# Optimization experiments

Hardware: AMD Instinct MI355X
Metric: run time of the kernel (lower is better)

Reference implementation:

```python
import jax, jax.numpy as jnp
import numpy as np

B, N, NNZ = 512, 512, 8192
ENTITY, EMB, HID = 30000, 64, 100
PAD_ID = ENTITY - 1


def setup_inputs() -> dict:
    key = jax.random.key(0)
    ks = jax.random.split(key, 8)
    hyperneigh = jax.random.randint(ks[0], (B, N), 0, PAD_ID, dtype=jnp.int64)
    adj_rows = jax.random.randint(ks[1], (B, NNZ), 0, N, dtype=jnp.int32)
    adj_cols = jax.random.randint(ks[2], (B, NNZ), 0, N, dtype=jnp.int32)
    adj_vals = jax.random.uniform(ks[3], (B, NNZ), dtype=jnp.float32)
    emb_table = jax.random.normal(ks[4], (ENTITY, EMB), dtype=jnp.float32)
    emb_table = emb_table.at[PAD_ID].set(0.0)  # padding_idx row is zero
    stdv1 = 1.0 / np.sqrt(HID)
    W1 = jax.random.uniform(ks[5], (EMB, HID), minval=-stdv1, maxval=stdv1, dtype=jnp.float32)
    b1 = jax.random.uniform(ks[6], (HID,), minval=-stdv1, maxval=stdv1, dtype=jnp.float32)
    k7, k8 = jax.random.split(ks[7])
    W2 = jax.random.uniform(k7, (HID, HID), minval=-stdv1, maxval=stdv1, dtype=jnp.float32)
    b2 = jax.random.uniform(k8, (HID,), minval=-stdv1, maxval=stdv1, dtype=jnp.float32)
    return dict(hyperneigh=hyperneigh, adj_rows=adj_rows, adj_cols=adj_cols,
                adj_vals=adj_vals, emb_table=emb_table, W1=W1, b1=b1, W2=W2, b2=b2)


def _spmm(rows, cols, vals, X):
    # sparse [N,N] @ X[N,H] via gather + segment_sum (COO, fixed nnz)
    msgs = vals[:, None] * X[cols]  # [nnz, H]
    return jax.ops.segment_sum(msgs, rows, num_segments=N)

_batched_spmm = jax.vmap(_spmm, in_axes=(0, 0, 0, 0))


def reference(hyperneigh, adj_rows, adj_cols, adj_vals, emb_table, W1, b1, W2, b2):
    # embedding lookup: [B, N, EMB]
    x = emb_table[hyperneigh]
    # HGNN_conv layer 1: support = X @ W; out = A @ support + bias
    support = jnp.einsum('bne,eh->bnh', x, W1)
    x = _batched_spmm(adj_rows, adj_cols, adj_vals, support) + b1
    # HGNN_conv layer 2
    support = jnp.einsum('bnh,hk->bnk', x, W2)
    x = _batched_spmm(adj_rows, adj_cols, adj_vals, support) + b2
    return x  # [B, N, HID]
```

## Files before the change

### kernel.cpp

```cpp
#include <hip/hip_runtime.h>

#define BB   512
#define NN   512
#define NNZ  8192
#define EMB  64
#define HID  100
#define DUMPC 512

#define OFF_CSR_RC  0
#define OFF_CSR_V   16777216
#define OFF_ROWST   25165824
#define OFF_SUPT    26216448
#define OFF_W1T     84936704
#define OFF_W2T     84951040

typedef __attribute__((ext_vector_type(8))) short short8;
typedef __attribute__((ext_vector_type(4))) float floatx4;

__device__ __forceinline__ unsigned short f2bf(float f) {
    unsigned u = __float_as_uint(f);
    unsigned r = (u + 0x7fffu + ((u >> 16) & 1u)) >> 16;
    return (unsigned short)r;
}

__device__ __forceinline__ short8 pack8(float4 a, float4 b) {
    short8 s;
    s[0] = (short)f2bf(a.x); s[1] = (short)f2bf(a.y);
    s[2] = (short)f2bf(a.z); s[3] = (short)f2bf(a.w);
    s[4] = (short)f2bf(b.x); s[5] = (short)f2bf(b.y);
    s[6] = (short)f2bf(b.z); s[7] = (short)f2bf(b.w);
    return s;
}

__device__ __forceinline__ size_t supt_addr(int batch, int col, int k) {
    return (size_t)batch * 57344 + (size_t)(k >> 5) * 3584 + (size_t)col * 32 + (k & 31);
}

__global__ __launch_bounds__(512) void k_csr_build(
    const int* __restrict__ rows, const int* __restrict__ cols,
    const float* __restrict__ vals, int* __restrict__ row_start,
    int* __restrict__ csr_rc, unsigned short* __restrict__ csr_v,
    const float* __restrict__ W1, const float* __restrict__ W2,
    unsigned short* __restrict__ w1t, unsigned short* __restrict__ w2t)
{
    __shared__ int   rl[NNZ];
    __shared__ float vl[NNZ];
    __shared__ int   cnt[NN];
    __shared__ int   sc[NN];

    const int b   = blockIdx.x;
    const int tid = threadIdx.x;

    if (b == BB) {
        for (int id = tid; id < 112 * 128; id += 512) {
            if (id < 112 * 64) {
                int h = id >> 6, k = id & 63;
                float f = (h < 100) ? W1[k * 100 + h] : 0.f;
                w1t[id] = f2bf(f);
            }
            int h = id >> 7, k = id & 127;
            float f = (h < 100 && k < 100) ? W2[k * 100 + h] : 0.f;
            w2t[id] = f2bf(f);
        }
        return;
    }

    const int*   rb = rows + (size_t)b * NNZ;
    const int*   cb = cols + (size_t)b * NNZ;
    const float* vb = vals + (size_t)b * NNZ;

    cnt[tid] = 0;
    __syncthreads();

    #pragma unroll
    for (int i = 0; i < NNZ / 512; ++i)
        atomicAdd(&cnt[rb[tid + i * 512]], 1);
    __syncthreads();

    const int own = cnt[tid];
    sc[tid] = own;
    __syncthreads();
    #pragma unroll
    for (int off = 1; off < NN; off <<= 1) {
        int v = (tid >= off) ? sc[tid - off] : 0;
        __syncthreads();
        sc[tid] += v;
        __syncthreads();
    }
    row_start[b * 513 + tid + 1] = sc[tid];
    if (tid == 0) row_start[b * 513] = 0;
    cnt[tid] = sc[tid] - own;
    __syncthreads();

    #pragma unroll
    for (int i = 0; i < NNZ / 512; ++i) {
        int idx = tid + i * 512;
        int   r = rb[idx];
        int   c = cb[idx];
        float v = vb[idx];
        int pos = atomicAdd(&cnt[r], 1);
        rl[pos] = (r << 16) | c;
        vl[pos] = v;
    }
    __syncthreads();

    {
        const int s = sc[tid] - own;
        const int e = sc[tid];
        for (int j = s; j < e - 1; ++j) {
            int pj = rl[j];
            if ((pj & 0xffff) == DUMPC) continue;
            float add = 0.f;
            bool mod = false;
            for (int j2 = j + 1; j2 < e; ++j2) {
                if (rl[j2] == pj) {
                    add += vl[j2];
                    rl[j2] = (pj & 0xffff0000) | DUMPC;
                    mod = true;
                }
            }
            if (mod) vl[j] += add;
        }
    }
    __syncthreads();

    #pragma unroll
    for (int i = 0; i < NNZ / 512; ++i) {
        int idx = tid + i * 512;
        csr_rc[(size_t)b * NNZ + idx] = rl[idx];
        csr_v [(size_t)b * NNZ + idx] = f2bf(vl[idx]);
    }
}

__global__ __launch_bounds__(256) void k_gemm1_mfma(
    const int* __restrict__ hyper, const float* __restrict__ emb,
    const unsigned short* __restrict__ w1t, unsigned short* __restrict__ supT)
{
    const int lane = threadIdx.x & 63, wave = threadIdx.x >> 6;
    const int l15 = lane & 15, g4 = lane >> 4;

    short8 bq[7][2];
    #pragma unroll
    for (int ct = 0; ct < 7; ++ct)
        #pragma unroll
        for (int kt = 0; kt < 2; ++kt)
            bq[ct][kt] = *(const short8*)(w1t + (ct * 16 + l15) * 64 + kt * 32 + g4 * 8);

    const int wsid = blockIdx.x * 4 + wave;
    #pragma unroll 2
    for (int i = 0; i < 4; ++i) {
        const int  rb   = wsid * 4 + i;
        const long base = (long)rb * 16;
        const int  rid  = hyper[base + l15];
        const float* ep = emb + (long)rid * EMB + g4 * 8;
        float4 f0 = *(const float4*)(ep);
        float4 f1 = *(const float4*)(ep + 4);
        float4 f2 = *(const float4*)(ep + 32);
        float4 f3 = *(const float4*)(ep + 36);
        short8 a0 = pack8(f0, f1);
        short8 a1 = pack8(f2, f3);

        floatx4 acc[7];
        #pragma unroll
        for (int ct = 0; ct < 7; ++ct) acc[ct] = (floatx4)0.f;
        #pragma unroll
        for (int ct = 0; ct < 7; ++ct) {
            acc[ct] = __builtin_amdgcn_mfma_f32_16x16x32_bf16(a0, bq[ct][0], acc[ct], 0, 0, 0);
            acc[ct] = __builtin_amdgcn_mfma_f32_16x16x32_bf16(a1, bq[ct][1], acc[ct], 0, 0, 0);
        }

        const int batch = rb >> 5;
        const int inrow = (rb & 31) * 16 + g4 * 4;
        #pragma unroll
        for (int ct = 0; ct < 7; ++ct) {
            int col = ct * 16 + l15;
            uint2 w;
            w.x = (unsigned)f2bf(acc[ct][0]) | ((unsigned)f2bf(acc[ct][1]) << 16);
            w.y = (unsigned)f2bf(acc[ct][2]) | ((unsigned)f2bf(acc[ct][3]) << 16);
            *(uint2*)(supT + supt_addr(batch, col, inrow)) = w;
        }
    }
}

__global__ __launch_bounds__(256) void k_gemm2_mfma(
    const unsigned short* __restrict__ h1, const unsigned short* __restrict__ w2t,
    unsigned short* __restrict__ supT)
{
    const int lane = threadIdx.x & 63, wave = threadIdx.x >> 6;
    const int l15 = lane & 15, g4 = lane >> 4;
    const int ct0 = (wave & 1) ? 4 : 0;

    short8 bq[4][4];
    #pragma unroll
    for (int ctl = 0; ctl < 4; ++ctl) {
        int ct = ct0 + ctl;
        if (ct < 7)
            #pragma unroll
            for (int kt = 0; kt < 4; ++kt)
                bq[ctl][kt] = *(const short8*)(w2t + (ct * 16 + l15) * 128 + kt * 32 + g4 * 8);
    }

    const int wp = blockIdx.x * 2 + (wave >> 1);
    #pragma unroll 2
    for (int i = 0; i < 8; ++i) {
        const int  rb   = wp * 8 + i;
        const long base = (long)rb * 16;
        const unsigned short* rp = h1 + (size_t)(base + l15) * 112;

        short8 a[4];
        #pragma unroll
        for (int kt = 0; kt < 4; ++kt) {
            int k0 = kt * 32 + g4 * 8;
            short8 av = (short8)(short)0;
            if (k0 < 112) av = *(const short8*)(rp + k0);
            a[kt] = av;
        }

        floatx4 acc[4];
        #pragma unroll
        for (int ctl = 0; ctl < 4; ++ctl) acc[ctl] = (floatx4)0.f;
        #pragma unroll
        for (int ctl = 0; ctl < 4; ++ctl) {
            if (ct0 + ctl < 7) {
                #pragma unroll
                for (int kt = 0; kt < 4; ++kt)
                    acc[ctl] = __builtin_amdgcn_mfma_f32_16x16x32_bf16(a[kt], bq[ctl][kt], acc[ctl], 0, 0, 0);
            }
        }

        const int batch = rb >> 5;
        const int inrow = (rb & 31) * 16 + g4 * 4;
        #pragma unroll
        for (int ctl = 0; ctl < 4; ++ctl) {
            if (ct0 + ctl < 7) {
                int col = (ct0 + ctl) * 16 + l15;
                uint2 w;
                w.x = (unsigned)f2bf(acc[ctl][0]) | ((unsigned)f2bf(acc[ctl][1]) << 16);
                w.y = (unsigned)f2bf(acc[ctl][2]) | ((unsigned)f2bf(acc[ctl][3]) << 16);
                *(uint2*)(supT + supt_addr(batch, col, inrow)) = w;
            }
        }
    }
}

template<bool FINAL>
__global__ __launch_bounds__(512) void k_spmm_mfma(
    const int* __restrict__ row_st, const int* __restrict__ rc,
    const unsigned short* __restrict__ vv, const unsigned short* __restrict__ supT,
    const float* __restrict__ bias, unsigned short* __restrict__ h1,
    float* __restrict__ out)
{
    __shared__ unsigned short Ad[64 * 512 + 64];

    const int tid    = threadIdx.x;
    const int xcd    = blockIdx.x & 7;
    const int local  = blockIdx.x >> 3;
    const int batch  = xcd * 64 + (local >> 3);
    const int stripe = local & 7;
    const int r0     = stripe * 64;

    const int s0 = row_st[batch * 513 + r0];
    const int e0 = row_st[batch * 513 + r0 + 64];
    const int*            rcb = rc + (size_t)batch * NNZ;
    const unsigned short* vvb = vv + (size_t)batch * NNZ;
    int            pc[3];
    unsigned short pv[3];
    #pragma unroll
    for (int i = 0; i < 3; ++i) {
        int idx = s0 + tid + i * 512;
        bool ok = idx < e0;
        pc[i] = ok ? rcb[idx] : 0;
        pv[i] = ok ? vvb[idx] : 0;
    }

    {
        uint4* z = (uint4*)Ad;
        #pragma unroll
        for (int i = 0; i < 9; ++i) {
            int idx = tid + i * 512;
            if (idx < 4104) z[idx] = make_uint4(0u, 0u, 0u, 0u);
        }
    }
    __syncthreads();

    #pragma unroll
    for (int i = 0; i < 3; ++i) {
        int idx = s0 + tid + i * 512;
        if (idx < e0) {
            int r = ((pc[i] >> 16) & 0xffff) - r0;
            int c = pc[i] & 0xffff;
            int a = (c < 512)
                ? ((r >> 4) * 8192 + (c >> 5) * 512 + ((c >> 3) & 3) * 128 + (r & 15) * 8 + (c & 7))
                : (64 * 512 + (tid & 63));
            Ad[a] = pv[i];
        }
    }
    for (int idx = s0 + 1536 + tid; idx < e0; idx += 512) {
        int p = rcb[idx];
        int r = ((p >> 16) & 0xffff) - r0;
        int c = p & 0xffff;
        int a = (c < 512)
            ? ((r >> 4) * 8192 + (c >> 5) * 512 + ((c >> 3) & 3) * 128 + (r & 15) * 8 + (c & 7))
            : (64 * 512 + (tid & 63));
        Ad[a] = vvb[idx];
    }
    __syncthreads();

    const int lane = tid & 63, wave = tid >> 6;
    const int l15 = lane & 15, g4 = lane >> 4;
    const int ng  = wave & 3, kh = wave >> 2;
    const int nt0 = ng * 2;
    const bool two = (nt0 + 1) < 7;
    const int ktb = kh * 8;

    const unsigned short* b0p = supT + (size_t)batch * 57344 + (size_t)ktb * 3584
                               + (nt0 * 16 + l15) * 32 + g4 * 8;
    const unsigned short* b1p = b0p + 512;
    const unsigned short* ap  = Ad + (size_t)ktb * 512 + lane * 8;

    floatx4 acc[2][4];
    #pragma unroll
    for (int n = 0; n < 2; ++n)
        #pragma unroll
        for (int m = 0; m < 4; ++m) acc[n][m] = (floatx4)0.f;

    #pragma unroll 4
    for (int kt = 0; kt < 8; ++kt) {
        short8 b0 = *(const short8*)(b0p + (size_t)kt * 3584);
        short8 b1 = (short8)(short)0;
        if (two) b1 = *(const short8*)(b1p + (size_t)kt * 3584);
        #pragma unroll
        for (int m = 0; m < 4; ++m) {
            short8 a = *(const short8*)(ap + m * 8192 + kt * 512);
            acc[0][m] = __builtin_amdgcn_mfma_f32_16x16x32_bf16(a, b0, acc[0][m], 0, 0, 0);
            if (two)
                acc[1][m] = __builtin_amdgcn_mfma_f32_16x16x32_bf16(a, b1, acc[1][m], 0, 0, 0);
        }
    }
    __syncthreads();

    float* redu = (float*)Ad;
    if (kh == 1) {
        #pragma unroll
        for (int nn = 0; nn < 2; ++nn)
            #pragma unroll
            for (int m = 0; m < 4; ++m)
                #pragma unroll
                for (int q = 0; q < 4; ++q)
                    redu[ng * 2048 + ((nn * 4 + m) * 4 + q) * 64 + lane] = acc[nn][m][q];
    }
    __syncthreads();

    if (kh == 0) {
        #pragma unroll
        for (int nn = 0; nn < 2; ++nn)
            #pragma unroll
            for (int m = 0; m < 4; ++m)
                #pragma unroll
                for (int q = 0; q < 4; ++q)
                    acc[nn][m][q] += redu[ng * 2048 + ((nn * 4 + m) * 4 + q) * 64 + lane];

        if (FINAL) {
            float* st = (float*)((char*)Ad + 32768);
            #pragma unroll
            for (int nn = 0; nn < 2; ++nn) {
                int nt = nt0 + nn;
                if (nt >= 7) break;
                int col = nt * 16 + l15;
                float bi = (col < HID) ? bias[col] : 0.f;
                #pragma unroll
                for (int m = 0; m < 4; ++m) {
                    int row = m * 16 + g4 * 4;
                    #pragma unroll
                    for (int q = 0; q < 4; ++q)
                        st[(row + q) * 112 + col] = acc[nn][m][q] + bi;
                }
            }
        } else {
            unsigned short* st = (unsigned short*)((char*)Ad + 32768);
            #pragma unroll
            for (int nn = 0; nn < 2; ++nn) {
                int nt = nt0 + nn;
                if (nt >= 7) break;
                int col = nt * 16 + l15;
                float bi = (col < HID) ? bias[col] : 0.f;
                #pragma unroll
                for (int m = 0; m < 4; ++m) {
                    int row = m * 16 + g4 * 4;
                    #pragma unroll
                    for (int q = 0; q < 4; ++q)
                        st[(row + q) * 112 + col] = f2bf(acc[nn][m][q] + bi);
                }
            }
        }
    }
    __syncthreads();

    if (FINAL) {
        const float* st = (const float*)((char*)Ad + 32768);
        #pragma unroll
        for (int i = 0; i < 4; ++i) {
            int flat = tid + i * 512;
            if (flat < 1600) {
                int row = flat / 25, wi = flat - row * 25;
                float4 v = *(const float4*)(st + row * 112 + wi * 4);
                *(float4*)(out + ((size_t)batch * NN + r0 + row) * HID + wi * 4) = v;
            }
        }
    } else {
        const unsigned short* st = (const unsigned short*)((char*)Ad + 32768);
        #pragma unroll
        for (int i = 0; i < 2; ++i) {
            int flat = tid + i * 512;
            if (flat < 896) {
                int row = flat / 14, wi = flat - row * 14;
                uint4 v = *(const uint4*)(st + row * 112 + wi * 8);
                *(uint4*)(h1 + ((size_t)batch * NN + r0 + row) * 112 + wi * 8) = v;
            }
        }
    }
}

extern "C" void kernel_launch(void* const* d_in, const int* in_sizes, int n_in,
                              void* d_out, int out_size, void* d_ws, size_t ws_size,
                              hipStream_t stream)
{
    const int*   hyper = (const int*)  d_in[0];
    const int*   arows = (const int*)  d_in[1];
    const int*   acols = (const int*)  d_in[2];
    const float* avals = (const float*)d_in[3];
    const float* emb   = (const float*)d_in[4];
    const float* W1    = (const float*)d_in[5];
    const float* b1    = (const float*)d_in[6];
    const float* W2    = (const float*)d_in[7];
    const float* b2    = (const float*)d_in[8];

    float*          out = (float*)d_out;
    unsigned short* h1  = (unsigned short*)d_out;
    char*           ws  = (char*)d_ws;

    int*            csr_rc = (int*)           (ws + OFF_CSR_RC);
    unsigned short* csr_v  = (unsigned short*)(ws + OFF_CSR_V);
    int*            row_st = (int*)           (ws + OFF_ROWST);
    unsigned short* supT   = (unsigned short*)(ws + OFF_SUPT);
    unsigned short* w1t    = (unsigned short*)(ws + OFF_W1T);
    unsigned short* w2t    = (unsigned short*)(ws + OFF_W2T);

    k_csr_build<<<BB + 1, 512, 0, stream>>>(arows, acols, avals, row_st,
                                            csr_rc, csr_v, W1, W2, w1t, w2t);

    k_gemm1_mfma<<<1024, 256, 0, stream>>>(hyper, emb, w1t, supT);
    k_spmm_mfma<false><<<BB * 8, 512, 0, stream>>>(row_st, csr_rc, csr_v, supT, b1, h1, out);
    k_gemm2_mfma<<<1024, 256, 0, stream>>>(h1, w2t, supT);
    k_spmm_mfma<true><<<BB * 8, 512, 0, stream>>>(row_st, csr_rc, csr_v, supT, b2, h1, out);
}
```

Measured before the change: 238.6 us.

## Detect duplicate COO entries with shared-memory bitmap and wave-shuffle prefix scan

Replaces the per-row quadratic duplicate-merge loop in CSR build with a per-(row,col) shared bitmap set by atomicOr. Duplicates are diverted to an exception list and folded into the first occurrence via atomicAdd. The block-wide Hillis-Steele scan with many barriers becomes a wave-level shuffle scan plus an 8-wave combine. The weight-transpose block moves to block 0. This adds 32KB of LDS per block, which may lower occupancy, and the exception list has a fixed cap.

```diff
diff --git a/kernel.cpp b/kernel.cpp
--- a/kernel.cpp
+++ b/kernel.cpp
@@ -6,6 +6,7 @@
 #define EMB  64
 #define HID  100
 #define DUMPC 512
+#define EXCAP 1024
 
 #define OFF_CSR_RC  0
 #define OFF_CSR_V   16777216
@@ -43,15 +44,18 @@
     const float* __restrict__ W1, const float* __restrict__ W2,
     unsigned short* __restrict__ w1t, unsigned short* __restrict__ w2t)
 {
-    __shared__ int   rl[NNZ];
-    __shared__ float vl[NNZ];
-    __shared__ int   cnt[NN];
-    __shared__ int   sc[NN];
-
-    const int b   = blockIdx.x;
+    __shared__ int      rl[NNZ];
+    __shared__ float    vl[NNZ];
+    __shared__ unsigned bmap[NN * 16];
+    __shared__ int      cnt[NN];
+    __shared__ int      sc[NN];
+    __shared__ int      exc_rc[EXCAP];
+    __shared__ float    exc_v[EXCAP];
+    __shared__ int      wsum[8], woff[8], nexc;
+
     const int tid = threadIdx.x;
 
-    if (b == BB) {
+    if (blockIdx.x == 0) {
         for (int id = tid; id < 112 * 128; id += 512) {
             if (id < 112 * 64) {
                 int h = id >> 6, k = id & 63;
@@ -64,12 +68,16 @@
         }
         return;
     }
+    const int b = blockIdx.x - 1;
 
     const int*   rb = rows + (size_t)b * NNZ;
     const int*   cb = cols + (size_t)b * NNZ;
     const float* vb = vals + (size_t)b * NNZ;
 
     cnt[tid] = 0;
+    #pragma unroll
+    for (int i = 0; i < 16; ++i) bmap[tid + i * 512] = 0u;
+    if (tid == 0) nexc = 0;
     __syncthreads();
 
     #pragma unroll
@@ -77,19 +85,27 @@
         atomicAdd(&cnt[rb[tid + i * 512]], 1);
     __syncthreads();
 
+    const int lane = tid & 63, wid = tid >> 6;
     const int own = cnt[tid];
-    sc[tid] = own;
-    __syncthreads();
-    #pragma unroll
-    for (int off = 1; off < NN; off <<= 1) {
-        int v = (tid >= off) ? sc[tid - off] : 0;
-        __syncthreads();
-        sc[tid] += v;
-        __syncthreads();
-    }
-    row_start[b * 513 + tid + 1] = sc[tid];
+    int x = own;
+    #pragma unroll
+    for (int off = 1; off < 64; off <<= 1) {
+        int y = __shfl_up(x, off);
+        if (lane >= off) x += y;
+    }
+    if (lane == 63) wsum[wid] = x;
+    __syncthreads();
+    if (tid == 0) {
+        int a = 0;
+        #pragma unroll
+        for (int w = 0; w < 8; ++w) { woff[w] = a; a += wsum[w]; }
+    }
+    __syncthreads();
+    x += woff[wid];
+    sc[tid] = x;
+    row_start[b * 513 + tid + 1] = x;
     if (tid == 0) row_start[b * 513] = 0;
-    cnt[tid] = sc[tid] - own;
+    cnt[tid] = x - own;
     __syncthreads();
 
     #pragma unroll
@@ -98,28 +114,34 @@
         int   r = rb[idx];
         int   c = cb[idx];
         float v = vb[idx];
+        unsigned bit = 1u << (c & 31);
+        unsigned old = atomicOr(&bmap[(r << 4) + (c >> 5)], bit);
         int pos = atomicAdd(&cnt[r], 1);
-        rl[pos] = (r << 16) | c;
-        vl[pos] = v;
+        bool dup = (old & bit) != 0;
+        int e = -1;
+        if (dup) e = atomicAdd(&nexc, 1);
+        if (dup && e < EXCAP) {
+            rl[pos] = (r << 16) | DUMPC;
+            vl[pos] = 0.f;
+            exc_rc[e] = (r << 16) | c;
+            exc_v[e]  = v;
+        } else {
+            rl[pos] = (r << 16) | c;
+            vl[pos] = v;
+        }
     }
     __syncthreads();
 
     {
-        const int s = sc[tid] - own;
-        const int e = sc[tid];
-        for (int j = s; j < e - 1; ++j) {
-            int pj = rl[j];
-            if ((pj & 0xffff) == DUMPC) continue;
-            float add = 0.f;
-            bool mod = false;
-            for (int j2 = j + 1; j2 < e; ++j2) {
-                if (rl[j2] == pj) {
-                    add += vl[j2];
-                    rl[j2] = (pj & 0xffff0000) | DUMPC;
-                    mod = true;
-                }
-            }
-            if (mod) vl[j] += add;
+        int ne = nexc < EXCAP ? nexc : EXCAP;
+        for (int t = tid; t < ne; t += 512) {
+            int key = exc_rc[t];
+            int r   = key >> 16;
+            int lo  = r ? sc[r - 1] : 0;
+            int hi  = sc[r];
+            for (int j = lo; j < hi; ++j) {
+                if (rl[j] == key) { atomicAdd(&vl[j], exc_v[t]); break; }
+            }
         }
     }
     __syncthreads();
```

After: 216.5 us. 9.2% less time.
